# Performance work log

Measured on AMD Instinct MI355X. Metric: run time of the kernel, lower is better.

## Reference

```python
import jax, jax.numpy as jnp
import numpy as np

DIM = 768
NUM_HEADS = 12
HEAD_DIM = 64
HIDDEN = NUM_HEADS * HEAD_DIM  # 768


def setup_inputs() -> dict:
    key = jax.random.key(0)
    k_x, k_qkv, k_proj = jax.random.split(key, 3)
    B, N = 8, 1024
    x = jax.random.normal(k_x, (B, N, DIM), dtype=jnp.float32)
    # nn.Linear(dim, 3*hidden, bias=False): weight [3*hidden, dim]; store transposed for x @ W
    W_qkv = jax.random.normal(k_qkv, (DIM, 3 * HIDDEN), dtype=jnp.float32) * (DIM ** -0.5)
    W_proj = jax.random.normal(k_proj, (HIDDEN, DIM), dtype=jnp.float32) * (HIDDEN ** -0.5)
    return {"x": x, "W_qkv": W_qkv, "W_proj": W_proj}


def reference(x, W_qkv, W_proj):
    B, N, C = x.shape
    scale = HEAD_DIM ** -0.5
    qkv = (x @ W_qkv).reshape(B, N, 3, NUM_HEADS, HEAD_DIM)
    qkv = jnp.transpose(qkv, (2, 0, 3, 1, 4))  # [3, B, H, N, D]
    q, k, v = qkv[0], qkv[1], qkv[2]
    attn = jnp.einsum('bhnd,bhmd->bhnm', q, k) * scale  # [B, H, N, N]
    attn = jax.nn.softmax(attn, axis=-1)
    out = jnp.einsum('bhnm,bhmd->bhnd', attn, v)  # [B, H, N, D]
    out = jnp.transpose(out, (0, 2, 1, 3)).reshape(B, N, HIDDEN)
    return out @ W_proj
```

## Files before the change

### kernel.cpp

```cpp
#include <hip/hip_runtime.h>
#include <cstdint>
#include <cstddef>

typedef __attribute__((ext_vector_type(8))) short bf16x8;
typedef __attribute__((ext_vector_type(4))) float f32x4;
typedef __attribute__((ext_vector_type(4))) unsigned short us4;
typedef __attribute__((ext_vector_type(8))) unsigned short us8;

#define NHEADS 12
#define BATCH 8
#define SEQ 1024
#define HDIM 64
#define CDIM 768
#define QKV_N 2304
#define BHND ((size_t)(BATCH) * NHEADS * SEQ * HDIM)
#define NX   ((size_t)8192 * 768)
#define NWQ  ((size_t)768 * 2304)
#define NWP  ((size_t)768 * 768)

__device__ __forceinline__ unsigned short f2bf(float f) {
    union { float f; uint32_t u; } v; v.f = f;
    uint32_t u = v.u;
    u += 0x7fffu + ((u >> 16) & 1u);
    return (unsigned short)(u >> 16);
}

__device__ __forceinline__ void gl_lds16(const unsigned short* g, unsigned short* l) {
    __builtin_amdgcn_global_load_lds(
        (const __attribute__((address_space(1))) void*)g,
        (__attribute__((address_space(3))) void*)l, 16, 0, 0);
}

__global__ __launch_bounds__(256) void conv_x(const float* __restrict__ in,
                                              unsigned short* __restrict__ out) {
    const size_t stride = (size_t)gridDim.x * blockDim.x;
    for (size_t i8 = (size_t)blockIdx.x * 256 + threadIdx.x; i8 < NX / 8; i8 += stride) {
        f32x4 a = *(const f32x4*)&in[i8 * 8];
        f32x4 b = *(const f32x4*)&in[i8 * 8 + 4];
        us8 o;
#pragma unroll
        for (int j = 0; j < 4; ++j) { o[j] = f2bf(a[j]); o[4 + j] = f2bf(b[j]); }
        *(us8*)&out[i8 * 8] = o;
    }
}

__global__ __launch_bounds__(256) void tconv(const float* __restrict__ in,
                                             unsigned short* __restrict__ out,
                                             int R, int C) {
    __shared__ unsigned short tile[64][68];
    const int bx = blockIdx.x * 64;
    const int by = blockIdx.y * 64;
    const int t = threadIdx.x;
    const int rr = t >> 4;
    const int c4 = (t & 15) * 4;
#pragma unroll
    for (int i = 0; i < 4; ++i) {
        const int r = rr + i * 16;
        f32x4 v = *(const f32x4*)&in[(size_t)(by + r) * C + bx + c4];
#pragma unroll
        for (int j = 0; j < 4; ++j) tile[c4 + j][r] = f2bf(v[j]);
    }
    __syncthreads();
#pragma unroll
    for (int i = 0; i < 4; ++i) {
        const int r = rr + i * 16;
        us4 o;
#pragma unroll
        for (int j = 0; j < 4; ++j) o[j] = tile[r][c4 + j];
        *(us4*)&out[(size_t)(bx + r) * R + by + c4] = o;
    }
}

__global__ __launch_bounds__(256) void qkv_gemm2(const unsigned short* __restrict__ A,
                                                 const unsigned short* __restrict__ BT,
                                                 unsigned short* __restrict__ qkv) {
    __shared__ unsigned short a_lds[128][32];
    __shared__ unsigned short b_lds[128][32];
    const int m0 = blockIdx.y * 128;
    const int n0 = blockIdx.x * 128;
    const int t = threadIdx.x, lane = t & 63, w = t >> 6;
    const int wm = w >> 1, wn = w & 1;
    const int lr = lane & 15, kg = lane >> 4;
    const int srow = w * 16 + (lane >> 2);
    const int scol = (lane & 3) * 8;

    f32x4 acc[4][4];
#pragma unroll
    for (int i = 0; i < 4; ++i)
#pragma unroll
        for (int j = 0; j < 4; ++j) acc[i][j] = (f32x4)0.f;

    unsigned short* ab0 = &a_lds[0][0] + w * 512;
    unsigned short* ab1 = &a_lds[0][0] + (4 + w) * 512;
    unsigned short* bb0 = &b_lds[0][0] + w * 512;
    unsigned short* bb1 = &b_lds[0][0] + (4 + w) * 512;

    for (int kt = 0; kt < 24; ++kt) {
        const int k0 = kt * 32;
        __syncthreads();
        gl_lds16(&A[(size_t)(m0 + srow) * CDIM + k0 + scol], ab0);
        gl_lds16(&A[(size_t)(m0 + 64 + srow) * CDIM + k0 + scol], ab1);
        gl_lds16(&BT[(size_t)(n0 + srow) * CDIM + k0 + scol], bb0);
        gl_lds16(&BT[(size_t)(n0 + 64 + srow) * CDIM + k0 + scol], bb1);
        __syncthreads();

        bf16x8 afr[4], bfr[4];
#pragma unroll
        for (int i = 0; i < 4; ++i)
            afr[i] = *(const bf16x8*)&a_lds[wm * 64 + i * 16 + lr][kg * 8];
#pragma unroll
        for (int j = 0; j < 4; ++j)
            bfr[j] = *(const bf16x8*)&b_lds[wn * 64 + j * 16 + lr][kg * 8];
#pragma unroll
        for (int i = 0; i < 4; ++i)
#pragma unroll
            for (int j = 0; j < 4; ++j)
                acc[i][j] = __builtin_amdgcn_mfma_f32_16x16x32_bf16(afr[i], bfr[j],
                                                                    acc[i][j], 0, 0, 0);
    }

#pragma unroll
    for (int j = 0; j < 4; ++j) {
        const int c = n0 + wn * 64 + j * 16 + lr;
        const int three = (c >= 1536) ? 2 : ((c >= 768) ? 1 : 0);
        const int rem = c - three * 768;
        const int h = rem >> 6, d = rem & 63;
        const float mul = (three == 0) ? 0.125f : 1.0f;
#pragma unroll
        for (int i = 0; i < 4; ++i) {
#pragma unroll
            for (int rg = 0; rg < 4; ++rg) {
                const int m = m0 + wm * 64 + i * 16 + kg * 4 + rg;
                const int bb = m >> 10, n = m & 1023;
                qkv[(size_t)three * BHND +
                    ((size_t)(bb * NHEADS + h) * SEQ + n) * HDIM + d] =
                    f2bf(acc[i][j][rg] * mul);
            }
        }
    }
}

__global__ __launch_bounds__(256) void attn_kernel3(const unsigned short* __restrict__ qkv,
                                                    unsigned short* __restrict__ aout) {
    __shared__ unsigned short v_lds[2][64][72];
    __shared__ unsigned short p_lds[4][2][16][72];
    const int bh = blockIdx.y;
    const int qt = blockIdx.x;
    const int t = threadIdx.x, lane = t & 63, w = t >> 6;
    const int lr = lane & 15, kg = lane >> 4;
    const unsigned short* Q = qkv + (size_t)bh * SEQ * HDIM;
    const unsigned short* K = qkv + BHND + (size_t)bh * SEQ * HDIM;
    const unsigned short* V = qkv + 2 * BHND + (size_t)bh * SEQ * HDIM;

    const int qA = qt * 128 + w * 32;
    bf16x8 qfA[2], qfB[2];
#pragma unroll
    for (int ks = 0; ks < 2; ++ks) {
        qfA[ks] = *(const bf16x8*)&Q[(size_t)(qA + lr) * HDIM + ks * 32 + kg * 8];
        qfB[ks] = *(const bf16x8*)&Q[(size_t)(qA + 16 + lr) * HDIM + ks * 32 + kg * 8];
    }

    const int skey = t >> 4, sd4 = (t & 15) * 4;
#pragma unroll
    for (int i = 0; i < 4; ++i) {
        const int key = skey + i * 16;
        us4 vvv = *(const us4*)&V[(size_t)key * HDIM + sd4];
#pragma unroll
        for (int j = 0; j < 4; ++j) v_lds[0][sd4 + j][key] = vvv[j];
    }
    __syncthreads();

    float mA = -1e30f, lA = 0.f, mB = -1e30f, lB = 0.f;
    f32x4 oaccA[4], oaccB[4];
#pragma unroll
    for (int jd = 0; jd < 4; ++jd) { oaccA[jd] = (f32x4)0.f; oaccB[jd] = (f32x4)0.f; }

    for (int kv = 0; kv < 16; ++kv) {
        const int kb = kv * 64;
        if (kv < 15) {
            const int buf = (kv + 1) & 1;
#pragma unroll
            for (int i = 0; i < 4; ++i) {
                const int key = skey + i * 16;
                us4 vvv = *(const us4*)&V[(size_t)(kb + 64 + key) * HDIM + sd4];
#pragma unroll
                for (int j = 0; j < 4; ++j) v_lds[buf][sd4 + j][key] = vvv[j];
            }
        }

        f32x4 sA[4], sB[4];
#pragma unroll
        for (int jj = 0; jj < 4; ++jj) {
            sA[jj] = (f32x4)0.f; sB[jj] = (f32x4)0.f;
#pragma unroll
            for (int ks = 0; ks < 2; ++ks) {
                bf16x8 kf = *(const bf16x8*)&K[(size_t)(kb + jj * 16 + lr) * HDIM + ks * 32 + kg * 8];
                sA[jj] = __builtin_amdgcn_mfma_f32_16x16x32_bf16(kf, qfA[ks], sA[jj], 0, 0, 0);
                sB[jj] = __builtin_amdgcn_mfma_f32_16x16x32_bf16(kf, qfB[ks], sB[jj], 0, 0, 0);
            }
        }

        {
            float m0 = fmaxf(fmaxf(sA[0][0], sA[0][1]), fmaxf(sA[0][2], sA[0][3]));
            float m1 = fmaxf(fmaxf(sA[1][0], sA[1][1]), fmaxf(sA[1][2], sA[1][3]));
            float m2 = fmaxf(fmaxf(sA[2][0], sA[2][1]), fmaxf(sA[2][2], sA[2][3]));
            float m3 = fmaxf(fmaxf(sA[3][0], sA[3][1]), fmaxf(sA[3][2], sA[3][3]));
            float mx = fmaxf(fmaxf(m0, m1), fmaxf(m2, m3));
            mx = fmaxf(mx, __shfl_xor(mx, 16, 64));
            mx = fmaxf(mx, __shfl_xor(mx, 32, 64));
            const float mnew = fmaxf(mA, mx);
            const float corr = __expf(mA - mnew);
            float rs = 0.f;
#pragma unroll
            for (int jj = 0; jj < 4; ++jj)
#pragma unroll
                for (int r = 0; r < 4; ++r) { sA[jj][r] = __expf(sA[jj][r] - mnew); rs += sA[jj][r]; }
            rs += __shfl_xor(rs, 16, 64);
            rs += __shfl_xor(rs, 32, 64);
            lA = lA * corr + rs; mA = mnew;
#pragma unroll
            for (int jd = 0; jd < 4; ++jd)
#pragma unroll
                for (int r = 0; r < 4; ++r) oaccA[jd][r] *= corr;
        }
        {
            float m0 = fmaxf(fmaxf(sB[0][0], sB[0][1]), fmaxf(sB[0][2], sB[0][3]));
            float m1 = fmaxf(fmaxf(sB[1][0], sB[1][1]), fmaxf(sB[1][2], sB[1][3]));
            float m2 = fmaxf(fmaxf(sB[2][0], sB[2][1]), fmaxf(sB[2][2], sB[2][3]));
            float m3 = fmaxf(fmaxf(sB[3][0], sB[3][1]), fmaxf(sB[3][2], sB[3][3]));
            float mx = fmaxf(fmaxf(m0, m1), fmaxf(m2, m3));
            mx = fmaxf(mx, __shfl_xor(mx, 16, 64));
            mx = fmaxf(mx, __shfl_xor(mx, 32, 64));
            const float mnew = fmaxf(mB, mx);
            const float corr = __expf(mB - mnew);
            float rs = 0.f;
#pragma unroll
            for (int jj = 0; jj < 4; ++jj)
#pragma unroll
                for (int r = 0; r < 4; ++r) { sB[jj][r] = __expf(sB[jj][r] - mnew); rs += sB[jj][r]; }
            rs += __shfl_xor(rs, 16, 64);
            rs += __shfl_xor(rs, 32, 64);
            lB = lB * corr + rs; mB = mnew;
#pragma unroll
            for (int jd = 0; jd < 4; ++jd)
#pragma unroll
                for (int r = 0; r < 4; ++r) oaccB[jd][r] *= corr;
        }

#pragma unroll
        for (int jj = 0; jj < 4; ++jj)
#pragma unroll
            for (int r = 0; r < 4; ++r) {
                p_lds[w][0][lr][jj * 16 + kg * 4 + r] = f2bf(sA[jj][r]);
                p_lds[w][1][lr][jj * 16 + kg * 4 + r] = f2bf(sB[jj][r]);
            }
        asm volatile("s_waitcnt lgkmcnt(0)" ::: "memory");
        __builtin_amdgcn_sched_barrier(0);

        const int cb = kv & 1;
#pragma unroll
        for (int c = 0; c < 2; ++c) {
            bf16x8 pfA = *(const bf16x8*)&p_lds[w][0][lr][c * 32 + kg * 8];
            bf16x8 pfB = *(const bf16x8*)&p_lds[w][1][lr][c * 32 + kg * 8];
#pragma unroll
            for (int jd = 0; jd < 4; ++jd) {
                bf16x8 vf = *(const bf16x8*)&v_lds[cb][jd * 16 + lr][c * 32 + kg * 8];
                oaccA[jd] = __builtin_amdgcn_mfma_f32_16x16x32_bf16(vf, pfA, oaccA[jd], 0, 0, 0);
                oaccB[jd] = __builtin_amdgcn_mfma_f32_16x16x32_bf16(vf, pfB, oaccB[jd], 0, 0, 0);
            }
        }

        __syncthreads();
    }

    const int bb = bh / NHEADS, h = bh % NHEADS;
    const float invA = 1.0f / lA, invB = 1.0f / lB;
#pragma unroll
    for (int jd = 0; jd < 4; ++jd) {
#pragma unroll
        for (int r = 0; r < 4; ++r) {
            const int d = jd * 16 + kg * 4 + r;
            aout[((size_t)(bb * SEQ + qA + lr)) * CDIM + h * HDIM + d] =
                f2bf(oaccA[jd][r] * invA);
            aout[((size_t)(bb * SEQ + qA + 16 + lr)) * CDIM + h * HDIM + d] =
                f2bf(oaccB[jd][r] * invB);
        }
    }
}

__global__ __launch_bounds__(256) void proj_gemm2(const unsigned short* __restrict__ A,
                                                  const unsigned short* __restrict__ BT,
                                                  float* __restrict__ out) {
    __shared__ unsigned short a_lds[128][32];
    __shared__ unsigned short b_lds[128][32];
    const int m0 = blockIdx.y * 128;
    const int n0 = blockIdx.x * 128;
    const int t = threadIdx.x, lane = t & 63, w = t >> 6;
    const int wm = w >> 1, wn = w & 1;
    const int lr = lane & 15, kg = lane >> 4;
    const int srow = w * 16 + (lane >> 2);
    const int scol = (lane & 3) * 8;

    f32x4 acc[4][4];
#pragma unroll
    for (int i = 0; i < 4; ++i)
#pragma unroll
        for (int j = 0; j < 4; ++j) acc[i][j] = (f32x4)0.f;

    unsigned short* ab0 = &a_lds[0][0] + w * 512;
    unsigned short* ab1 = &a_lds[0][0] + (4 + w) * 512;
    unsigned short* bb0 = &b_lds[0][0] + w * 512;
    unsigned short* bb1 = &b_lds[0][0] + (4 + w) * 512;

    for (int kt = 0; kt < 24; ++kt) {
        const int k0 = kt * 32;
        __syncthreads();
        gl_lds16(&A[(size_t)(m0 + srow) * CDIM + k0 + scol], ab0);
        gl_lds16(&A[(size_t)(m0 + 64 + srow) * CDIM + k0 + scol], ab1);
        gl_lds16(&BT[(size_t)(n0 + srow) * CDIM + k0 + scol], bb0);
        gl_lds16(&BT[(size_t)(n0 + 64 + srow) * CDIM + k0 + scol], bb1);
        __syncthreads();

        bf16x8 afr[4], bfr[4];
#pragma unroll
        for (int i = 0; i < 4; ++i)
            afr[i] = *(const bf16x8*)&a_lds[wm * 64 + i * 16 + lr][kg * 8];
#pragma unroll
        for (int j = 0; j < 4; ++j)
            bfr[j] = *(const bf16x8*)&b_lds[wn * 64 + j * 16 + lr][kg * 8];
#pragma unroll
        for (int i = 0; i < 4; ++i)
#pragma unroll
            for (int j = 0; j < 4; ++j)
                acc[i][j] = __builtin_amdgcn_mfma_f32_16x16x32_bf16(afr[i], bfr[j],
                                                                    acc[i][j], 0, 0, 0);
    }

#pragma unroll
    for (int i = 0; i < 4; ++i)
#pragma unroll
        for (int j = 0; j < 4; ++j)
#pragma unroll
            for (int rg = 0; rg < 4; ++rg) {
                const int m = m0 + wm * 64 + i * 16 + kg * 4 + rg;
                const int c = n0 + wn * 64 + j * 16 + lr;
                out[(size_t)m * CDIM + c] = acc[i][j][rg];
            }
}

extern "C" void kernel_launch(void* const* d_in, const int* in_sizes, int n_in,
                              void* d_out, int out_size, void* d_ws, size_t ws_size,
                              hipStream_t stream) {
    const float* x      = (const float*)d_in[0];
    const float* w_qkv  = (const float*)d_in[1];
    const float* w_proj = (const float*)d_in[2];

    unsigned short* qkv  = (unsigned short*)d_ws;
    unsigned short* aout = qkv + 3 * BHND;
    unsigned short* xb   = aout + NX;
    unsigned short* wqt  = xb + NX;
    unsigned short* wpt  = wqt + NWQ;
    float* out = (float*)d_out;

    conv_x<<<2048, 256, 0, stream>>>(x, xb);
    tconv<<<dim3(QKV_N / 64, CDIM / 64), 256, 0, stream>>>(w_qkv, wqt, CDIM, QKV_N);
    tconv<<<dim3(CDIM / 64, CDIM / 64), 256, 0, stream>>>(w_proj, wpt, CDIM, CDIM);
    qkv_gemm2<<<dim3(18, 64), 256, 0, stream>>>(xb, wqt, qkv);
    attn_kernel3<<<dim3(8, 96), 256, 0, stream>>>(qkv, aout);
    proj_gemm2<<<dim3(6, 64), 256, 0, stream>>>(aout, wpt, out);
}
```

Measured before the change: 163.3 us.

## Swizzle V and P LDS tiles, vectorize P stores, skip unneeded softmax rescale

XOR-swizzles the columns of the transposed V tile and the per-wave P tile in shared memory to reduce bank conflicts on the scattered writes and the 16-byte MFMA operand reads. P is now written as 4-element vectors instead of scalar stores. The online-softmax correction of the output accumulators and running sum is skipped when no lane's row maximum increased. This adds index arithmetic and a wave-uniform branch.

```diff
diff --git a/kernel.cpp b/kernel.cpp
--- a/kernel.cpp
+++ b/kernel.cpp
@@ -140,7 +140,7 @@
     }
 }
 
-__global__ __launch_bounds__(256) void attn_kernel3(const unsigned short* __restrict__ qkv,
+__global__ __launch_bounds__(256) void attn_kernel4(const unsigned short* __restrict__ qkv,
                                                     unsigned short* __restrict__ aout) {
     __shared__ unsigned short v_lds[2][64][72];
     __shared__ unsigned short p_lds[4][2][16][72];
@@ -161,12 +161,18 @@
     }
 
     const int skey = t >> 4, sd4 = (t & 15) * 4;
+    const int vswz = ((t & 15) >> 1) * 8;
+    const int pswz = ((lr >> 1) & 7) * 8;
+    int vrswz[4];
+#pragma unroll
+    for (int jd = 0; jd < 4; ++jd) vrswz[jd] = ((jd * 2 + (lr >> 3)) & 7) * 8;
+
 #pragma unroll
     for (int i = 0; i < 4; ++i) {
         const int key = skey + i * 16;
         us4 vvv = *(const us4*)&V[(size_t)key * HDIM + sd4];
 #pragma unroll
-        for (int j = 0; j < 4; ++j) v_lds[0][sd4 + j][key] = vvv[j];
+        for (int j = 0; j < 4; ++j) v_lds[0][sd4 + j][key ^ vswz] = vvv[j];
     }
     __syncthreads();
 
@@ -184,7 +190,7 @@
                 const int key = skey + i * 16;
                 us4 vvv = *(const us4*)&V[(size_t)(kb + 64 + key) * HDIM + sd4];
 #pragma unroll
-                for (int j = 0; j < 4; ++j) v_lds[buf][sd4 + j][key] = vvv[j];
+                for (int j = 0; j < 4; ++j) v_lds[buf][sd4 + j][key ^ vswz] = vvv[j];
             }
         }
 
@@ -209,7 +215,6 @@
             mx = fmaxf(mx, __shfl_xor(mx, 16, 64));
             mx = fmaxf(mx, __shfl_xor(mx, 32, 64));
             const float mnew = fmaxf(mA, mx);
-            const float corr = __expf(mA - mnew);
             float rs = 0.f;
 #pragma unroll
             for (int jj = 0; jj < 4; ++jj)
@@ -217,11 +222,16 @@
                 for (int r = 0; r < 4; ++r) { sA[jj][r] = __expf(sA[jj][r] - mnew); rs += sA[jj][r]; }
             rs += __shfl_xor(rs, 16, 64);
             rs += __shfl_xor(rs, 32, 64);
-            lA = lA * corr + rs; mA = mnew;
-#pragma unroll
-            for (int jd = 0; jd < 4; ++jd)
-#pragma unroll
-                for (int r = 0; r < 4; ++r) oaccA[jd][r] *= corr;
+            if (__any(mx > mA)) {
+                const float corr = __expf(mA - mnew);
+                lA = lA * corr + rs; mA = mnew;
+#pragma unroll
+                for (int jd = 0; jd < 4; ++jd)
+#pragma unroll
+                    for (int r = 0; r < 4; ++r) oaccA[jd][r] *= corr;
+            } else {
+                lA += rs;
+            }
         }
         {
             float m0 = fmaxf(fmaxf(sB[0][0], sB[0][1]), fmaxf(sB[0][2], sB[0][3]));
@@ -232,7 +242,6 @@
             mx = fmaxf(mx, __shfl_xor(mx, 16, 64));
             mx = fmaxf(mx, __shfl_xor(mx, 32, 64));
             const float mnew = fmaxf(mB, mx);
-            const float corr = __expf(mB - mnew);
             float rs = 0.f;
 #pragma unroll
             for (int jj = 0; jj < 4; ++jj)
@@ -240,31 +249,40 @@
                 for (int r = 0; r < 4; ++r) { sB[jj][r] = __expf(sB[jj][r] - mnew); rs += sB[jj][r]; }
             rs += __shfl_xor(rs, 16, 64);
             rs += __shfl_xor(rs, 32, 64);
-            lB = lB * corr + rs; mB = mnew;
-#pragma unroll
-            for (int jd = 0; jd < 4; ++jd)
-#pragma unroll
-                for (int r = 0; r < 4; ++r) oaccB[jd][r] *= corr;
-        }
-
-#pragma unroll
-        for (int jj = 0; jj < 4; ++jj)
-#pragma unroll
-            for (int r = 0; r < 4; ++r) {
-                p_lds[w][0][lr][jj * 16 + kg * 4 + r] = f2bf(sA[jj][r]);
-                p_lds[w][1][lr][jj * 16 + kg * 4 + r] = f2bf(sB[jj][r]);
-            }
+            if (__any(mx > mB)) {
+                const float corr = __expf(mB - mnew);
+                lB = lB * corr + rs; mB = mnew;
+#pragma unroll
+                for (int jd = 0; jd < 4; ++jd)
+#pragma unroll
+                    for (int r = 0; r < 4; ++r) oaccB[jd][r] *= corr;
+            } else {
+                lB += rs;
+            }
+        }
+
+#pragma unroll
+        for (int jj = 0; jj < 4; ++jj) {
+            us4 oa, ob;
+#pragma unroll
+            for (int r = 0; r < 4; ++r) { oa[r] = f2bf(sA[jj][r]); ob[r] = f2bf(sB[jj][r]); }
+            const int col = (jj * 16 + kg * 4) ^ pswz;
+            *(us4*)&p_lds[w][0][lr][col] = oa;
+            *(us4*)&p_lds[w][1][lr][col] = ob;
+        }
         asm volatile("s_waitcnt lgkmcnt(0)" ::: "memory");
         __builtin_amdgcn_sched_barrier(0);
 
         const int cb = kv & 1;
 #pragma unroll
         for (int c = 0; c < 2; ++c) {
-            bf16x8 pfA = *(const bf16x8*)&p_lds[w][0][lr][c * 32 + kg * 8];
-            bf16x8 pfB = *(const bf16x8*)&p_lds[w][1][lr][c * 32 + kg * 8];
+            const int pcol = (c * 32 + kg * 8) ^ pswz;
+            bf16x8 pfA = *(const bf16x8*)&p_lds[w][0][lr][pcol];
+            bf16x8 pfB = *(const bf16x8*)&p_lds[w][1][lr][pcol];
 #pragma unroll
             for (int jd = 0; jd < 4; ++jd) {
-                bf16x8 vf = *(const bf16x8*)&v_lds[cb][jd * 16 + lr][c * 32 + kg * 8];
+                const int vcol = (c * 32 + kg * 8) ^ vrswz[jd];
+                bf16x8 vf = *(const bf16x8*)&v_lds[cb][jd * 16 + lr][vcol];
                 oaccA[jd] = __builtin_amdgcn_mfma_f32_16x16x32_bf16(vf, pfA, oaccA[jd], 0, 0, 0);
                 oaccB[jd] = __builtin_amdgcn_mfma_f32_16x16x32_bf16(vf, pfB, oaccB[jd], 0, 0, 0);
             }
@@ -366,6 +384,6 @@
     tconv<<<dim3(QKV_N / 64, CDIM / 64), 256, 0, stream>>>(w_qkv, wqt, CDIM, QKV_N);
     tconv<<<dim3(CDIM / 64, CDIM / 64), 256, 0, stream>>>(w_proj, wpt, CDIM, CDIM);
     qkv_gemm2<<<dim3(18, 64), 256, 0, stream>>>(xb, wqt, qkv);
-    attn_kernel3<<<dim3(8, 96), 256, 0, stream>>>(qkv, aout);
+    attn_kernel4<<<dim3(8, 96), 256, 0, stream>>>(qkv, aout);
     proj_gemm2<<<dim3(6, 64), 256, 0, stream>>>(aout, wpt, out);
 }
```

Result: slower. 231.6 us (+41.8%).
